# Kernel tuning notes

Hardware: AMD Instinct MI355X
Metric: run time of the kernel (lower is better)

Reference implementation:

```python
import jax, jax.numpy as jnp
import numpy as np


def softcap(x, a=10.0):
    return a * jnp.tanh(x / a)


def setup_inputs() -> dict:
    key = jax.random.key(0)
    B, T, D = 4, 2048, 256
    ks = jax.random.split(key, 5)
    w = lambda k, s: jax.random.normal(k, s, dtype=jnp.float32) * 0.02
    return {
        "x": jax.random.normal(ks[0], (B, T, D), dtype=jnp.float32),
        "Wq": w(ks[1], (D, D)),
        "bq": jnp.zeros((D,), jnp.float32),
        "Wk": w(ks[2], (D, D)),
        "bk": jnp.zeros((D,), jnp.float32),
        "Wv": w(ks[3], (D, D)),
        "bv": jnp.zeros((D,), jnp.float32),
        "Wg": w(ks[4], (D, 3 * D)),
        "bg": jnp.zeros((3 * D,), jnp.float32),
        "input_bias": -jnp.ones((D,), jnp.float32),   # Constant(-1.0) init
        "norm_scale": jnp.ones((D,), jnp.float32),    # RMSNorm scale
    }


def reference(x, Wq, bq, Wk, bk, Wv, bv, Wg, bg, input_bias, norm_scale):
    B, T, D = x.shape
    inv_sqrt_d = 1.0 / jnp.sqrt(jnp.asarray(D, jnp.float32))

    # Projections over all timesteps at once (time-parallel part).
    q = x @ Wq + bq                      # [B,T,D]
    k = (x @ Wk + bk) * inv_sqrt_d       # [B,T,D]
    v = x @ Wv + bv                      # [B,T,D]
    gates = x @ Wg + bg                  # [B,T,3D]
    i_pre, f_pre, o_pre = jnp.split(gates, 3, axis=-1)
    log_i = softcap(i_pre + input_bias)  # [B,T,D]
    log_f = -jax.nn.softplus(f_pre)      # [B,T,D]

    def step(carry, inp):
        M, n, m = carry                  # M:[B,D,D], n:[B,D], m:[B,D]
        qt, kt, vt, li, lf, op = inp     # each [B,D]
        m_next = jnp.maximum(lf + m, li)
        i_s = jnp.exp(li - m_next)
        f_s = jnp.exp(lf + m - m_next)
        M = f_s[:, :, None] * M + i_s[:, :, None] * (vt[:, :, None] * kt[:, None, :])
        n = f_s * n + i_s * kt
        h_raw = jnp.einsum('bij,bj->bi', M, qt)
        denom = jnp.maximum(jnp.abs(jnp.einsum('bi,bi->b', n, qt))[:, None], 1e-6)
        h = jax.nn.sigmoid(op) * (h_raw / denom)
        return (M, n, m_next), h

    M0 = jnp.zeros((B, D, D), jnp.float32)
    n0 = jnp.zeros((B, D), jnp.float32)
    m0 = jnp.zeros((B, D), jnp.float32)
    xs = tuple(jnp.swapaxes(a, 0, 1) for a in (q, k, v, log_i, log_f, o_pre))  # [T,B,D]
    _, hs = jax.lax.scan(step, (M0, n0, m0), xs)
    out = jnp.swapaxes(hs, 0, 1)         # [B,T,D]

    # RMSNorm (eps=1e-8); dropout is identity in eval mode.
    rms = jnp.sqrt(jnp.mean(out * out, axis=-1, keepdims=True) + 1e-8)
    return out / rms * norm_scale
```

## Files before the change

kernel.cpp:

```cpp
#include <hip/hip_runtime.h>
#include <hip/hip_bf16.h>
#include <math.h>

#define T_LEN 2048
#define BATCH 4
#define DMODEL 256
#define MROWS (BATCH*T_LEN)
#define PLANE (MROWS*DMODEL)
#define CH_L 32
#define NCH  (T_LEN/CH_L)
#define SUMSZ (BATCH*NCH*DMODEL)
#define MSLOT (DMODEL*DMODEL)

typedef __bf16 bf16;
typedef __bf16 bf16x4 __attribute__((ext_vector_type(4)));
typedef __bf16 bf16x8 __attribute__((ext_vector_type(8)));
typedef _Float16 f16;
typedef _Float16 f16x8 __attribute__((ext_vector_type(8)));
typedef float  f32x4  __attribute__((ext_vector_type(4)));
typedef unsigned short u16;
typedef u16 u16x8 __attribute__((ext_vector_type(8)));
typedef unsigned int u32;

#define MFMA(a,b,c)   __builtin_amdgcn_mfma_f32_16x16x32_bf16(a, b, c, 0, 0, 0)
#define MFMA16(a,b,c) __builtin_amdgcn_mfma_f32_16x16x32_f16(a, b, c, 0, 0, 0)

__device__ __forceinline__ void split_bf16(float x, bf16& hi, bf16& lo) {
    hi = (bf16)x;
    lo = (bf16)(x - (float)hi);
}

__device__ __forceinline__ float tanh_fast(float z) {
    z = fminf(fmaxf(z, -15.f), 15.f);
    float e = __expf(2.f * z);
    return (e - 1.f) / (e + 1.f);
}
__device__ __forceinline__ float nsoftplus_fast(float y) {
    return -(fmaxf(y, 0.f) + __logf(1.f + __expf(-fabsf(y))));
}
__device__ __forceinline__ float sigmoid_fast(float y) {
    return 1.f / (1.f + __expf(-y));
}

#define GLD16(SRC, DST) __builtin_amdgcn_global_load_lds( \
    (const __attribute__((address_space(1))) void*)(SRC), \
    (__attribute__((address_space(3))) void*)(DST), 16, 0, 0)

__global__ __launch_bounds__(256) void prep(const float* __restrict__ x,
                                            const float* __restrict__ Wq,
                                            const float* __restrict__ Wk,
                                            const float* __restrict__ Wv,
                                            const float* __restrict__ Wg,
                                            const float* __restrict__ bq,
                                            const float* __restrict__ bk,
                                            const float* __restrict__ bv,
                                            const float* __restrict__ bg,
                                            const float* __restrict__ input_bias,
                                            f16* __restrict__ xf,
                                            f16* __restrict__ Wf,
                                            float* __restrict__ biasC) {
    __shared__ float tile[16][260];
    const int tid = threadIdx.x;
    if (blockIdx.x < 1024) {
        int i = (blockIdx.x*256 + tid) * 8;
        f32x4 a = *(const f32x4*)(x + i);
        f32x4 b = *(const f32x4*)(x + i + 4);
        f16x8 h;
        #pragma unroll
        for (int e = 0; e < 4; ++e) {
            h[e]   = (f16)a[e];
            h[4+e] = (f16)b[e];
        }
        *(f16x8*)(xf + i) = h;
        return;
    }
    const int n0 = (blockIdx.x - 1024) * 16;
    const float* src; int nb, nw;
    float scale = 1.0f;
    if (n0 < 256)      { src = Wq; nb = n0;       nw = 256; }
    else if (n0 < 512) { src = Wk; nb = n0 - 256; nw = 256; scale = 0.0625f; }
    else if (n0 < 768) { src = Wv; nb = n0 - 512; nw = 256; }
    else               { src = Wg; nb = n0 - 768; nw = 768; }
    const int j = tid & 15, kk = tid >> 4;
    #pragma unroll
    for (int r = 0; r < 16; ++r) {
        int k = r*16 + kk;
        tile[j][k] = src[(size_t)k*nw + nb + j] * scale;
    }
    __syncthreads();
    #pragma unroll
    for (int r = 0; r < 16; ++r)
        Wf[(size_t)(n0 + r)*256 + tid] = (f16)tile[r][tid];
    if (tid < 16) {
        int n = n0 + tid;
        float bC;
        if (n < 256)        bC = bq[n];
        else if (n < 512)   bC = bk[n-256] * 0.0625f;
        else if (n < 768)   bC = bv[n-512];
        else if (n < 1024)  bC = bg[n-768] + input_bias[n-768];
        else                bC = bg[n-768];
        biasC[n] = bC;
    }
}

__global__ __launch_bounds__(256, 4) void proj_gemm(
    const f16* __restrict__ xf, const f16* __restrict__ Wf,
    const float* __restrict__ biasC,
    f16* __restrict__ qP, f16* __restrict__ kP, f16* __restrict__ vP,
    f16* __restrict__ liP, f16* __restrict__ lfP, f16* __restrict__ soP)
{
    __shared__ f16 Af[128*64];
    __shared__ f16 Bf[128*64];
    const int tid = threadIdx.x;
    const int w = tid >> 6, l = tid & 63;
    const int wr = w >> 1, wc = w & 1;
    const int m0 = blockIdx.x * 128;
    const int n0 = blockIdx.y * 128;
    const int lr = l & 15, lk = l >> 4;

    f32x4 acc[4][4] = {};

    for (int kt = 0; kt < 256; kt += 64) {
        #pragma unroll
        for (int p = 0; p < 4; ++p) {
            int e = p*2048 + tid*8;
            int row = e >> 6;
            int slot = (e >> 3) & 7;
            int scol = ((slot ^ (row & 7)) << 3);
            GLD16(xf + (size_t)(m0 + row)*256 + kt + scol, Af + e);
            GLD16(Wf + (size_t)(n0 + row)*256 + kt + scol, Bf + e);
        }
        __syncthreads();

        #pragma unroll
        for (int ksub = 0; ksub < 2; ++ksub) {
            f16x8 af[4], bf[4];
            #pragma unroll
            for (int mi = 0; mi < 4; ++mi) {
                int row = wr*64 + mi*16 + lr;
                int slot = (ksub*4 + lk) ^ (row & 7);
                af[mi] = *(const f16x8*)(Af + row*64 + slot*8);
            }
            #pragma unroll
            for (int ni = 0; ni < 4; ++ni) {
                int row = wc*64 + ni*16 + lr;
                int slot = (ksub*4 + lk) ^ (row & 7);
                bf[ni] = *(const f16x8*)(Bf + row*64 + slot*8);
            }
            #pragma unroll
            for (int ni = 0; ni < 4; ++ni)
                #pragma unroll
                for (int mi = 0; mi < 4; ++mi)
                    acc[mi][ni] = MFMA16(af[mi], bf[ni], acc[mi][ni]);
        }
        __syncthreads();
    }

    const int seg = n0 >> 8;
    f16* dst = (seg == 0) ? qP : (seg == 1) ? kP : (seg == 2) ? vP
             : (seg == 3) ? liP : (seg == 4) ? lfP : soP;
    #pragma unroll
    for (int mi = 0; mi < 4; ++mi) {
        #pragma unroll
        for (int ni = 0; ni < 4; ++ni) {
            int gcol = n0 + wc*64 + ni*16 + lr;
            int c = gcol & 255;
            float bC = biasC[gcol];
            #pragma unroll
            for (int r = 0; r < 4; ++r) {
                int grow = m0 + wr*64 + mi*16 + lk*4 + r;
                dst[(size_t)grow*256 + c] = (f16)(acc[mi][ni][r] + bC);
            }
        }
    }
}

__global__ __launch_bounds__(256) void s2_dm(
    const f16* __restrict__ kP, const f16* __restrict__ vP,
    const f16* __restrict__ liP, const f16* __restrict__ lfP,
    float* __restrict__ Csum, float* __restrict__ Mu, float* __restrict__ Bn,
    bf16* __restrict__ DM)
{
    __shared__ bf16 BTh[DMODEL][40], BTl[DMODEL][40];
    __shared__ bf16 KTh[DMODEL][40], KTl[DMODEL][40];
    const int tid = threadIdx.x;
    const int w = tid >> 6, l = tid & 63;
    const int b = blockIdx.x >> 6, c = blockIdx.x & 63;
    const size_t pb = ((size_t)b*T_LEN + (size_t)c*CH_L)*DMODEL;

    {
        float C = 0.f, mu = -3e38f;
        float val[CH_L];
        #pragma unroll
        for (int s = 0; s < CH_L; ++s) {
            size_t o = pb + (size_t)s*DMODEL + tid;
            C += nsoftplus_fast((float)lfP[o]);
            val[s] = 10.0f * tanh_fast(0.1f * (float)liP[o]) - C;
            mu = fmaxf(mu, val[s]);
        }
        float bn = 0.f;
        #pragma unroll
        for (int s = 0; s < CH_L; ++s) {
            size_t o = pb + (size_t)s*DMODEL + tid;
            float e = __expf(val[s] - mu);
            float kv = (float)kP[o];
            bn += e * kv;
            float bv = e * (float)vP[o];
            bf16 h, lo; split_bf16(bv, h, lo);
            BTh[tid][s] = h; BTl[tid][s] = lo;
            bf16 kh, kl; split_bf16(kv, kh, kl);
            KTh[tid][s] = kh; KTl[tid][s] = kl;
        }
        size_t so = ((size_t)b*NCH + c)*DMODEL + tid;
        Csum[so] = C; Mu[so] = mu; Bn[so] = bn;
    }
    __syncthreads();

    const int lr = l & 15, lk = l >> 4;
    bf16x8 Ah[4], Al[4];
    #pragma unroll
    for (int it = 0; it < 4; ++it) {
        int row = w*64 + it*16 + lr;
        Ah[it] = *(const bf16x8*)&BTh[row][lk*8];
        Al[it] = *(const bf16x8*)&BTl[row][lk*8];
    }
    bf16* DMc = DM + (size_t)((size_t)b*NCH + c)*MSLOT;
    #pragma unroll
    for (int jt = 0; jt < 16; ++jt) {
        int jcol = jt*16 + lr;
        bf16x8 bh = *(const bf16x8*)&KTh[jcol][lk*8];
        bf16x8 bl = *(const bf16x8*)&KTl[jcol][lk*8];
        #pragma unroll
        for (int it = 0; it < 4; ++it) {
            f32x4 a = {0.f,0.f,0.f,0.f};
            a = MFMA(Ah[it], bh, a);
            a = MFMA(Al[it], bh, a);
            a = MFMA(Ah[it], bl, a);
            #pragma unroll
            for (int r = 0; r < 4; ++r)
                DMc[(size_t)(w*64 + it*16 + lk*4 + r)*DMODEL + jcol] = (bf16)a[r];
        }
    }
}

__global__ __launch_bounds__(256) void chunk_compose(
    const float* __restrict__ Csum, const float* __restrict__ Mu, const float* __restrict__ Bn,
    float* __restrict__ mIn, float* __restrict__ nIn, float* __restrict__ Th,
    float* __restrict__ Dd, float* __restrict__ Ee)
{
    const int b = blockIdx.x;
    const int j = threadIdx.x;
    float m = 0.f, n = 0.f;
    #pragma unroll 1
    for (int c = 0; c < NCH; c += 4) {
        size_t o0 = ((size_t)b*NCH + c)*DMODEL + j;
        float cs0 = Csum[o0],            mu0 = Mu[o0],            bn0 = Bn[o0];
        float cs1 = Csum[o0 + DMODEL],   mu1 = Mu[o0 + DMODEL],   bn1 = Bn[o0 + DMODEL];
        float cs2 = Csum[o0 + 2*DMODEL], mu2 = Mu[o0 + 2*DMODEL], bn2 = Bn[o0 + 2*DMODEL];
        float cs3 = Csum[o0 + 3*DMODEL], mu3 = Mu[o0 + 3*DMODEL], bn3 = Bn[o0 + 3*DMODEL];
        #define STEP(CS, MUv, BNv, OFF) { \
            mIn[o0 + (OFF)] = m; nIn[o0 + (OFF)] = n; \
            float th = fmaxf(m, MUv); \
            Th[o0 + (OFF)] = th; \
            float emu = __expf(MUv - th); \
            float d = __expf(m - th); \
            Dd[o0 + (OFF)] = d; Ee[o0 + (OFF)] = emu; \
            n = d*n + emu*(BNv); \
            m = (CS) + th; }
        STEP(cs0, mu0, bn0, 0)
        STEP(cs1, mu1, bn1, DMODEL)
        STEP(cs2, mu2, bn2, 2*DMODEL)
        STEP(cs3, mu3, bn3, 3*DMODEL)
        #undef STEP
    }
}

__global__ __launch_bounds__(512) void s3_compose(
    const float* __restrict__ Dd, const float* __restrict__ Ee, bf16* __restrict__ DM)
{
    const int b = blockIdx.x >> 7;
    const int i = ((blockIdx.x & 127) << 1) + (threadIdx.x >> 8);
    const int j = threadIdx.x & 255;
    float acc = 0.f;
    const size_t base = ((size_t)b*NCH)*MSLOT + (size_t)i*DMODEL + j;
    const size_t sb = (size_t)b*NCH*DMODEL + i;
    #pragma unroll 1
    for (int c = 0; c < NCH; c += 4) {
        float dm0 = (float)DM[base + (size_t)(c+0)*MSLOT];
        float dm1 = (float)DM[base + (size_t)(c+1)*MSLOT];
        float dm2 = (float)DM[base + (size_t)(c+2)*MSLOT];
        float dm3 = (float)DM[base + (size_t)(c+3)*MSLOT];
        float d0 = Dd[sb + (size_t)(c+0)*DMODEL], e0 = Ee[sb + (size_t)(c+0)*DMODEL];
        float d1 = Dd[sb + (size_t)(c+1)*DMODEL], e1 = Ee[sb + (size_t)(c+1)*DMODEL];
        float d2 = Dd[sb + (size_t)(c+2)*DMODEL], e2 = Ee[sb + (size_t)(c+2)*DMODEL];
        float d3 = Dd[sb + (size_t)(c+3)*DMODEL], e3 = Ee[sb + (size_t)(c+3)*DMODEL];
        if (c > 0) DM[base + (size_t)(c+0)*MSLOT] = (bf16)acc;
        acc = d0*acc + e0*dm0;
        DM[base + (size_t)(c+1)*MSLOT] = (bf16)acc;
        acc = d1*acc + e1*dm1;
        DM[base + (size_t)(c+2)*MSLOT] = (bf16)acc;
        acc = d2*acc + e2*dm2;
        DM[base + (size_t)(c+3)*MSLOT] = (bf16)acc;
        acc = d3*acc + e3*dm3;
    }
}

__global__ __launch_bounds__(256) void s4_chunk(
    const f16* __restrict__ qP, const f16* __restrict__ kP, const f16* __restrict__ vP,
    const f16* __restrict__ liP, const f16* __restrict__ lfP, const f16* __restrict__ soP,
    const float* __restrict__ mIn, const float* __restrict__ nIn, const float* __restrict__ Th,
    const bf16* __restrict__ DM, const float* __restrict__ norm_scale,
    float* __restrict__ out)
{
    __shared__ __align__(16) char kqbuf[33792];
    bf16 (*Kf)[264] = (bf16(*)[264])kqbuf;
    bf16 (*Qf)[264] = (bf16(*)[264])(kqbuf + 16896);
    float (*Hout)[264] = (float(*)[264])kqbuf;
    __shared__ bf16 F1L[CH_L][264];
    __shared__ __align__(16) bf16 BTh[DMODEL][40];
    __shared__ __align__(16) bf16 GT[CH_L][48];
    __shared__ float part[CH_L][4];
    __shared__ float denoms[CH_L];
    __shared__ float exL[DMODEL];

    const int tid = threadIdx.x;
    const int w = tid >> 6, l = tid & 63;
    const int b = blockIdx.x >> 6;
    const int c = blockIdx.x & 63;
    const size_t pb = ((size_t)b*T_LEN + (size_t)c*CH_L)*DMODEL;

    const int i = tid;
    const size_t cbx = ((size_t)b*NCH + c)*DMODEL + i;
    const float thL = Th[cbx];
    const float mI = mIn[cbx];
    float P[CH_L];
    {
        float C = 0.f, mu = -3e38f, n = nIn[cbx], thp = mI;
        #pragma unroll
        for (int t = 0; t < CH_L; ++t) {
            size_t o = pb + (size_t)t*DMODEL + i;
            float lf = nsoftplus_fast((float)lfP[o]);
            float li = 10.0f * tanh_fast(0.1f * (float)liP[o]);
            float kv = (float)kP[o], qv = (float)qP[o], vv = (float)vP[o];
            C += lf;
            float vlc = li - C;
            mu = fmaxf(mu, vlc);
            float tht = fmaxf(mI, mu);
            float f = __expf(thp - tht);
            float iv = __expf(vlc - tht);
            n = f*n + iv*kv;
            thp = tht;
            P[t] = n * qv;
            Kf[t][i] = (bf16)kv;
            Qf[t][i] = (bf16)qv;
            F1L[t][i] = (bf16)__expf(mI - tht);
            BTh[i][t] = (bf16)(__expf(vlc - thL) * vv);
        }
        exL[i] = __expf(thL - mI);
    }
    #pragma unroll
    for (int t = 0; t < CH_L; ++t) {
        float s = P[t];
        #pragma unroll
        for (int sh = 32; sh; sh >>= 1) s += __shfl_xor(s, sh);
        if (l == 0) part[t][w] = s;
    }
    __syncthreads();

    if (tid < CH_L)
        denoms[tid] = fmaxf(fabsf(part[tid][0] + part[tid][1] + part[tid][2] + part[tid][3]), 1e-6f);

    {
        const int a = w & 1, bb = w >> 1;
        const int lr = l & 15, lk2 = l >> 4;
        if (a == 1 && bb == 0) {
            bf16x4 z = {(bf16)0.f, (bf16)0.f, (bf16)0.f, (bf16)0.f};
            *(bf16x4*)&GT[lr][16 + lk2*4] = z;
        } else {
            f32x4 g = {0.f,0.f,0.f,0.f};
            #pragma unroll
            for (int ks = 0; ks < 8; ++ks) {
                bf16x8 ah = *(const bf16x8*)&Kf[16*a  + lr][ks*32 + lk2*8];
                bf16x8 bh = *(const bf16x8*)&Qf[16*bb + lr][ks*32 + lk2*8];
                g = MFMA(ah, bh, g);
            }
            bf16x4 gv;
            #pragma unroll
            for (int r = 0; r < 4; ++r) {
                int s = 16*a + lk2*4 + r, t = 16*bb + lr;
                gv[r] = (s <= t) ? (bf16)g[r] : (bf16)0.f;
            }
            *(bf16x4*)&GT[16*bb + lr][16*a + lk2*4] = gv;
        }
    }
    __syncthreads();

    const int tt = w & 1;
    const int lr = l & 15, lk2 = l >> 4;
    const int trow = tt*16 + lr;
    f32x4 acc_a[8], acc_b[8];

    {
        bf16x8 gh = *(const bf16x8*)&GT[trow][lk2*8];
        #pragma unroll
        for (int it = 0; it < 8; ++it) {
            int irow = ((w>>1)*8 + it)*16 + lr;
            bf16x8 bb2 = *(const bf16x8*)&BTh[irow][lk2*8];
            f32x4 a = {0.f,0.f,0.f,0.f};
            acc_a[it] = MFMA(gh, bb2, a);
        }
    }
    #pragma unroll
    for (int it = 0; it < 8; ++it) acc_b[it] = (f32x4){0.f,0.f,0.f,0.f};
    if (c > 0) {
        const u16* Mbase = (const u16*)DM + (size_t)((size_t)b*NCH + c)*MSLOT;
        #pragma unroll
        for (int ks = 0; ks < 8; ++ks) {
            bf16x8 qh = *(const bf16x8*)&Qf[trow][ks*32 + lk2*8];
            #pragma unroll
            for (int it = 0; it < 8; ++it) {
                int irow = ((w>>1)*8 + it)*16 + lr;
                union { u16x8 u; bf16x8 h; } M8;
                M8.u = *(const u16x8*)(Mbase + (size_t)irow*DMODEL + ks*32 + lk2*8);
                acc_b[it] = MFMA(qh, M8.h, acc_b[it]);
            }
        }
    }
    __syncthreads();

    #pragma unroll
    for (int it = 0; it < 8; ++it) {
        int icol = ((w>>1)*8 + it)*16 + lr;
        float ex = exL[icol];
        #pragma unroll
        for (int r = 0; r < 4; ++r) {
            int t = tt*16 + lk2*4 + r;
            float F1 = (float)F1L[t][icol];
            float h = F1 * (acc_b[it][r] + ex * acc_a[it][r]);
            size_t o = pb + (size_t)t*DMODEL + icol;
            Hout[t][icol] = sigmoid_fast((float)soP[o]) * h / denoms[t];
        }
    }
    __syncthreads();
    #pragma unroll
    for (int r = 0; r < 8; ++r) {
        int t = w*8 + r;
        f32x4 hv = *(const f32x4*)&Hout[t][l*4];
        float ss = hv[0]*hv[0] + hv[1]*hv[1] + hv[2]*hv[2] + hv[3]*hv[3];
        #pragma unroll
        for (int sh = 32; sh; sh >>= 1) ss += __shfl_xor(ss, sh);
        float rinv = rsqrtf(ss * (1.0f/256.0f) + 1e-8f);
        f32x4 ns = *(const f32x4*)(norm_scale + l*4);
        f32x4 o4;
        #pragma unroll
        for (int e = 0; e < 4; ++e) o4[e] = hv[e] * rinv * ns[e];
        *(f32x4*)(out + pb + (size_t)t*DMODEL + l*4) = o4;
    }
}

extern "C" void kernel_launch(void* const* d_in, const int* in_sizes, int n_in,
                              void* d_out, int out_size, void* d_ws, size_t ws_size,
                              hipStream_t stream) {
    const float* x          = (const float*)d_in[0];
    const float* Wq         = (const float*)d_in[1];
    const float* bq         = (const float*)d_in[2];
    const float* Wk         = (const float*)d_in[3];
    const float* bk         = (const float*)d_in[4];
    const float* Wv         = (const float*)d_in[5];
    const float* bv         = (const float*)d_in[6];
    const float* Wg         = (const float*)d_in[7];
    const float* bg         = (const float*)d_in[8];
    const float* input_bias = (const float*)d_in[9];
    const float* norm_scale = (const float*)d_in[10];
    float* out = (float*)d_out;

    float* Csum = (float*)d_ws;
    float* Mu   = Csum + SUMSZ;
    float* Bn   = Mu   + SUMSZ;
    float* mIn  = Bn   + SUMSZ;
    float* nIn  = mIn  + SUMSZ;
    float* Th   = nIn  + SUMSZ;
    float* Dd   = Th   + SUMSZ;
    float* Ee   = Dd   + SUMSZ;
    float* biasC = Ee  + SUMSZ;
    f16*   qP   = (f16*)(biasC + 2048);
    f16*   kP   = qP  + PLANE;
    f16*   vP   = kP  + PLANE;
    f16*   liP  = vP  + PLANE;
    f16*   lfP  = liP + PLANE;
    f16*   soP  = lfP + PLANE;
    bf16*  DM   = (bf16*)(soP + PLANE);
    f16*   Wf   = (f16*)(DM + (size_t)BATCH*NCH*MSLOT);
    f16*   xf   = Wf + 1536*256;

    prep<<<dim3(1120), dim3(256), 0, stream>>>(x, Wq, Wk, Wv, Wg, bq, bk, bv, bg, input_bias,
                                               xf, Wf, biasC);
    proj_gemm<<<dim3(64, 12), dim3(256), 0, stream>>>(xf, Wf, biasC,
                                                      qP, kP, vP, liP, lfP, soP);
    s2_dm<<<dim3(BATCH*NCH), dim3(256), 0, stream>>>(kP, vP, liP, lfP, Csum, Mu, Bn, DM);
    chunk_compose<<<dim3(BATCH), dim3(256), 0, stream>>>(Csum, Mu, Bn, mIn, nIn, Th, Dd, Ee);
    s3_compose<<<dim3(BATCH*128), dim3(512), 0, stream>>>(Dd, Ee, DM);
    s4_chunk<<<dim3(BATCH*NCH), dim3(256), 0, stream>>>(qP, kP, vP, liP, lfP, soP,
                                                        mIn, nIn, Th, DM, norm_scale, out);
}
```

Measured before the change: 92.34 us.

## Fuse chunk summary, scalar compose and state scan into one sequential kernel

Replaces the three kernels (per-chunk DM via MFMA, per-batch chunk_compose, and the cross-chunk scan over DM) with one kernel. Each block owns two state rows and walks all chunks in order: one wavefront computes the gate prefix sums, max and normalizer with shuffles, then all threads update their two M rows in fp32 from k and write the chunk-start state. This removes the DM read-modify-write round trip and two launches, but serializes 64 chunks per block behind a barrier and replaces the MFMA work with scalar FMAs that reread k from global memory.

```diff
diff --git a/kernel.cpp b/kernel.cpp
--- a/kernel.cpp
+++ b/kernel.cpp
@@ -175,133 +175,79 @@
     }
 }
 
-__global__ __launch_bounds__(256) void s2_dm(
+__global__ __launch_bounds__(256) void s23(
     const f16* __restrict__ kP, const f16* __restrict__ vP,
     const f16* __restrict__ liP, const f16* __restrict__ lfP,
-    float* __restrict__ Csum, float* __restrict__ Mu, float* __restrict__ Bn,
+    float* __restrict__ mIn, float* __restrict__ nIn, float* __restrict__ Th,
     bf16* __restrict__ DM)
 {
-    __shared__ bf16 BTh[DMODEL][40], BTl[DMODEL][40];
-    __shared__ bf16 KTh[DMODEL][40], KTl[DMODEL][40];
+    __shared__ float bhat[2][64];
+    __shared__ float dscal[2][2];
     const int tid = threadIdx.x;
-    const int w = tid >> 6, l = tid & 63;
-    const int b = blockIdx.x >> 6, c = blockIdx.x & 63;
-    const size_t pb = ((size_t)b*T_LEN + (size_t)c*CH_L)*DMODEL;
-
-    {
-        float C = 0.f, mu = -3e38f;
-        float val[CH_L];
-        #pragma unroll
-        for (int s = 0; s < CH_L; ++s) {
-            size_t o = pb + (size_t)s*DMODEL + tid;
-            C += nsoftplus_fast((float)lfP[o]);
-            val[s] = 10.0f * tanh_fast(0.1f * (float)liP[o]) - C;
-            mu = fmaxf(mu, val[s]);
-        }
-        float bn = 0.f;
-        #pragma unroll
-        for (int s = 0; s < CH_L; ++s) {
-            size_t o = pb + (size_t)s*DMODEL + tid;
-            float e = __expf(val[s] - mu);
+    const int wv = tid >> 6, l = tid & 63;
+    const int b = blockIdx.x >> 7;
+    const int i0 = (blockIdx.x & 127) << 1;
+    const int j = tid;
+    const int g = l >> 5;
+    const int s = l & 31;
+    const int idim = i0 + g;
+
+    float M0 = 0.f, M1 = 0.f;
+    float m_st = 0.f, n_st = 0.f;
+
+    for (int c = 0; c < NCH; ++c) {
+        const int par = c & 1;
+        const size_t pb = ((size_t)b*T_LEN + (size_t)c*CH_L)*DMODEL;
+
+        {
+            bf16* DMc = DM + (size_t)((size_t)b*NCH + c)*MSLOT;
+            DMc[(size_t)i0*DMODEL + j]     = (bf16)M0;
+            DMc[(size_t)(i0+1)*DMODEL + j] = (bf16)M1;
+        }
+
+        if (wv == 0) {
+            size_t o = pb + (size_t)s*DMODEL + idim;
+            float lf = nsoftplus_fast((float)lfP[o]);
+            float li = 10.0f * tanh_fast(0.1f * (float)liP[o]);
             float kv = (float)kP[o];
-            bn += e * kv;
-            float bv = e * (float)vP[o];
-            bf16 h, lo; split_bf16(bv, h, lo);
-            BTh[tid][s] = h; BTl[tid][s] = lo;
-            bf16 kh, kl; split_bf16(kv, kh, kl);
-            KTh[tid][s] = kh; KTl[tid][s] = kl;
-        }
-        size_t so = ((size_t)b*NCH + c)*DMODEL + tid;
-        Csum[so] = C; Mu[so] = mu; Bn[so] = bn;
-    }
-    __syncthreads();
-
-    const int lr = l & 15, lk = l >> 4;
-    bf16x8 Ah[4], Al[4];
-    #pragma unroll
-    for (int it = 0; it < 4; ++it) {
-        int row = w*64 + it*16 + lr;
-        Ah[it] = *(const bf16x8*)&BTh[row][lk*8];
-        Al[it] = *(const bf16x8*)&BTl[row][lk*8];
-    }
-    bf16* DMc = DM + (size_t)((size_t)b*NCH + c)*MSLOT;
-    #pragma unroll
-    for (int jt = 0; jt < 16; ++jt) {
-        int jcol = jt*16 + lr;
-        bf16x8 bh = *(const bf16x8*)&KTh[jcol][lk*8];
-        bf16x8 bl = *(const bf16x8*)&KTl[jcol][lk*8];
-        #pragma unroll
-        for (int it = 0; it < 4; ++it) {
-            f32x4 a = {0.f,0.f,0.f,0.f};
-            a = MFMA(Ah[it], bh, a);
-            a = MFMA(Al[it], bh, a);
-            a = MFMA(Ah[it], bl, a);
-            #pragma unroll
-            for (int r = 0; r < 4; ++r)
-                DMc[(size_t)(w*64 + it*16 + lk*4 + r)*DMODEL + jcol] = (bf16)a[r];
-        }
-    }
-}
-
-__global__ __launch_bounds__(256) void chunk_compose(
-    const float* __restrict__ Csum, const float* __restrict__ Mu, const float* __restrict__ Bn,
-    float* __restrict__ mIn, float* __restrict__ nIn, float* __restrict__ Th,
-    float* __restrict__ Dd, float* __restrict__ Ee)
-{
-    const int b = blockIdx.x;
-    const int j = threadIdx.x;
-    float m = 0.f, n = 0.f;
-    #pragma unroll 1
-    for (int c = 0; c < NCH; c += 4) {
-        size_t o0 = ((size_t)b*NCH + c)*DMODEL + j;
-        float cs0 = Csum[o0],            mu0 = Mu[o0],            bn0 = Bn[o0];
-        float cs1 = Csum[o0 + DMODEL],   mu1 = Mu[o0 + DMODEL],   bn1 = Bn[o0 + DMODEL];
-        float cs2 = Csum[o0 + 2*DMODEL], mu2 = Mu[o0 + 2*DMODEL], bn2 = Bn[o0 + 2*DMODEL];
-        float cs3 = Csum[o0 + 3*DMODEL], mu3 = Mu[o0 + 3*DMODEL], bn3 = Bn[o0 + 3*DMODEL];
-        #define STEP(CS, MUv, BNv, OFF) { \
-            mIn[o0 + (OFF)] = m; nIn[o0 + (OFF)] = n; \
-            float th = fmaxf(m, MUv); \
-            Th[o0 + (OFF)] = th; \
-            float emu = __expf(MUv - th); \
-            float d = __expf(m - th); \
-            Dd[o0 + (OFF)] = d; Ee[o0 + (OFF)] = emu; \
-            n = d*n + emu*(BNv); \
-            m = (CS) + th; }
-        STEP(cs0, mu0, bn0, 0)
-        STEP(cs1, mu1, bn1, DMODEL)
-        STEP(cs2, mu2, bn2, 2*DMODEL)
-        STEP(cs3, mu3, bn3, 3*DMODEL)
-        #undef STEP
-    }
-}
-
-__global__ __launch_bounds__(512) void s3_compose(
-    const float* __restrict__ Dd, const float* __restrict__ Ee, bf16* __restrict__ DM)
-{
-    const int b = blockIdx.x >> 7;
-    const int i = ((blockIdx.x & 127) << 1) + (threadIdx.x >> 8);
-    const int j = threadIdx.x & 255;
-    float acc = 0.f;
-    const size_t base = ((size_t)b*NCH)*MSLOT + (size_t)i*DMODEL + j;
-    const size_t sb = (size_t)b*NCH*DMODEL + i;
-    #pragma unroll 1
-    for (int c = 0; c < NCH; c += 4) {
-        float dm0 = (float)DM[base + (size_t)(c+0)*MSLOT];
-        float dm1 = (float)DM[base + (size_t)(c+1)*MSLOT];
-        float dm2 = (float)DM[base + (size_t)(c+2)*MSLOT];
-        float dm3 = (float)DM[base + (size_t)(c+3)*MSLOT];
-        float d0 = Dd[sb + (size_t)(c+0)*DMODEL], e0 = Ee[sb + (size_t)(c+0)*DMODEL];
-        float d1 = Dd[sb + (size_t)(c+1)*DMODEL], e1 = Ee[sb + (size_t)(c+1)*DMODEL];
-        float d2 = Dd[sb + (size_t)(c+2)*DMODEL], e2 = Ee[sb + (size_t)(c+2)*DMODEL];
-        float d3 = Dd[sb + (size_t)(c+3)*DMODEL], e3 = Ee[sb + (size_t)(c+3)*DMODEL];
-        if (c > 0) DM[base + (size_t)(c+0)*MSLOT] = (bf16)acc;
-        acc = d0*acc + e0*dm0;
-        DM[base + (size_t)(c+1)*MSLOT] = (bf16)acc;
-        acc = d1*acc + e1*dm1;
-        DM[base + (size_t)(c+2)*MSLOT] = (bf16)acc;
-        acc = d2*acc + e2*dm2;
-        DM[base + (size_t)(c+3)*MSLOT] = (bf16)acc;
-        acc = d3*acc + e3*dm3;
+            float vv = (float)vP[o];
+            float C = lf;
+            #pragma unroll
+            for (int dlt = 1; dlt < 32; dlt <<= 1) {
+                float up = __shfl_up(C, dlt, 32);
+                if (s >= dlt) C += up;
+            }
+            float val = li - C;
+            float mu = val;
+            #pragma unroll
+            for (int m2 = 16; m2; m2 >>= 1) mu = fmaxf(mu, __shfl_xor(mu, m2, 32));
+            float e = __expf(val - mu);
+            float bk = e * kv;
+            #pragma unroll
+            for (int m2 = 16; m2; m2 >>= 1) bk += __shfl_xor(bk, m2, 32);
+            float Ct = __shfl(C, 31, 32);
+            float th  = fmaxf(m_st, mu);
+            float d   = __expf(m_st - th);
+            float emu = __expf(mu - th);
+            if (s == 0) {
+                size_t so = ((size_t)b*NCH + c)*DMODEL + idim;
+                mIn[so] = m_st; nIn[so] = n_st; Th[so] = th;
+                dscal[par][g] = d;
+            }
+            n_st = d*n_st + emu*bk;
+            m_st = Ct + th;
+            bhat[par][g*32 + s] = emu * e * vv;
+        }
+        __syncthreads();
+
+        const float d0 = dscal[par][0], d1 = dscal[par][1];
+        M0 *= d0; M1 *= d1;
+        #pragma unroll
+        for (int ss = 0; ss < CH_L; ++ss) {
+            float kf = (float)kP[pb + (size_t)ss*DMODEL + j];
+            M0 += bhat[par][ss]      * kf;
+            M1 += bhat[par][32 + ss] * kf;
+        }
     }
 }
 
@@ -474,15 +420,10 @@
     const float* norm_scale = (const float*)d_in[10];
     float* out = (float*)d_out;
 
-    float* Csum = (float*)d_ws;
-    float* Mu   = Csum + SUMSZ;
-    float* Bn   = Mu   + SUMSZ;
-    float* mIn  = Bn   + SUMSZ;
-    float* nIn  = mIn  + SUMSZ;
-    float* Th   = nIn  + SUMSZ;
-    float* Dd   = Th   + SUMSZ;
-    float* Ee   = Dd   + SUMSZ;
-    float* biasC = Ee  + SUMSZ;
+    float* mIn  = (float*)d_ws;
+    float* nIn  = mIn + SUMSZ;
+    float* Th   = nIn + SUMSZ;
+    float* biasC = Th + SUMSZ;
     f16*   qP   = (f16*)(biasC + 2048);
     f16*   kP   = qP  + PLANE;
     f16*   vP   = kP  + PLANE;
@@ -497,9 +438,7 @@
                                                xf, Wf, biasC);
     proj_gemm<<<dim3(64, 12), dim3(256), 0, stream>>>(xf, Wf, biasC,
                                                       qP, kP, vP, liP, lfP, soP);
-    s2_dm<<<dim3(BATCH*NCH), dim3(256), 0, stream>>>(kP, vP, liP, lfP, Csum, Mu, Bn, DM);
-    chunk_compose<<<dim3(BATCH), dim3(256), 0, stream>>>(Csum, Mu, Bn, mIn, nIn, Th, Dd, Ee);
-    s3_compose<<<dim3(BATCH*128), dim3(512), 0, stream>>>(Dd, Ee, DM);
+    s23<<<dim3(BATCH*128), dim3(256), 0, stream>>>(kP, vP, liP, lfP, mIn, nIn, Th, DM);
     s4_chunk<<<dim3(BATCH*NCH), dim3(256), 0, stream>>>(qP, kP, vP, liP, lfP, soP,
                                                         mIn, nIn, Th, DM, norm_scale, out);
 }
```

After: 162.5 us. 76.0% more time.
